# Kernel optimization log

Measured on AMD Instinct MI355X. Metric: run time of the kernel, lower is better.

The kernel has to match this reference:

```python
import jax, jax.numpy as jnp
import numpy as np

B, T = 64, 512          # batch, input_size
VOCAB = 16              # Embedding(16, ...)
UNITS = 256             # embedding dim
H = 512                 # LSTM hidden units (hard-coded in module)
F = 64                  # num_features (dense output)


def _glorot(key, shape):
    lim = np.sqrt(6.0 / (shape[0] + shape[1]))
    return jax.random.uniform(key, shape, jnp.float32, -lim, lim)


def setup_inputs() -> dict:
    key = jax.random.key(0)
    ks = jax.random.split(key, 9)
    tokens = jax.random.randint(ks[0], (B, T), 0, VOCAB, dtype=jnp.int32)
    return {
        "tokens": tokens,
        "emb": _glorot(ks[1], (VOCAB, UNITS)),
        "W1": _glorot(ks[2], (UNITS, 4 * H)),
        "U1": _glorot(ks[3], (H, 4 * H)),
        "b1": jnp.zeros((4 * H,), jnp.float32),
        "W2": _glorot(ks[4], (H, 4 * H)),
        "U2": _glorot(ks[5], (H, 4 * H)),
        "b2": jnp.zeros((4 * H,), jnp.float32),
        "Wd": _glorot(ks[6], (H, F)),
        "bd": jnp.zeros((F,), jnp.float32),
    }


def _lstm(x, mask, W, U, b, return_sequences):
    # x: [B, T, D]; mask: [B, T] bool. Keras semantics: masked steps carry
    # previous h and c (state and output pass through unchanged).
    xT = jnp.swapaxes(x, 0, 1)      # [T, B, D]
    mT = jnp.swapaxes(mask, 0, 1)   # [T, B]
    h0 = jnp.zeros((x.shape[0], U.shape[0]), x.dtype)
    c0 = h0

    def step(carry, inp):
        h, c = carry
        xt, mt = inp
        z = xt @ W + h @ U + b                    # [B, 4H]
        i, f, g, o = jnp.split(z, 4, axis=-1)     # Keras gate order i,f,c,o
        i = jax.nn.sigmoid(i)
        f = jax.nn.sigmoid(f)
        o = jax.nn.sigmoid(o)
        c_new = f * c + i * jnp.tanh(g)
        h_new = o * jnp.tanh(c_new)
        m = mt[:, None]
        h_new = jnp.where(m, h_new, h)
        c_new = jnp.where(m, c_new, c)
        return (h_new, c_new), h_new

    (h_last, _), hs = jax.lax.scan(step, (h0, c0), (xT, mT))
    return jnp.swapaxes(hs, 0, 1) if return_sequences else h_last


def reference(tokens, emb, W1, U1, b1, W2, U2, b2, Wd, bd):
    mask = tokens != 0                 # mask_zero=True
    x = emb[tokens]                    # [B, T, UNITS]
    h1 = _lstm(x, mask, W1, U1, b1, return_sequences=True)   # [B, T, H]
    h2 = _lstm(h1, mask, W2, U2, b2, return_sequences=False)  # [B, H]
    return h2 @ Wd + bd                # [B, F]
```

## Files before the change

### kernel.cpp

```cpp
#include <hip/hip_runtime.h>

#define BB   64
#define TT   512
#define NVOC 16
#define KIN  256
#define HH   512
#define GG   2048
#define FF   64

#define NWG  256
#define NTHR 512
#define WGPG 64
#define NGRP 4
#define BPG  16

#define TAB1_OFF 0
#define H1_OFF   32768
#define H2_OFF   98304

__device__ __forceinline__ void wg_barrier(unsigned* ctr, unsigned target) {
  __syncthreads();
  if (threadIdx.x == 0) {
    __hip_atomic_fetch_add(ctr, 1u, __ATOMIC_RELEASE, __HIP_MEMORY_SCOPE_AGENT);
    while (__hip_atomic_load(ctr, __ATOMIC_ACQUIRE, __HIP_MEMORY_SCOPE_AGENT) < target) {
      __builtin_amdgcn_s_sleep(2);
    }
  }
  __syncthreads();
}

extern "C" __global__ void __launch_bounds__(NTHR, 2)
lstm_fused(const int* __restrict__ tokens, const float* __restrict__ emb,
           const float* __restrict__ W1, const float* __restrict__ U1,
           const float* __restrict__ b1, const float* __restrict__ W2,
           const float* __restrict__ U2, const float* __restrict__ b2,
           const float* __restrict__ Wd, const float* __restrict__ bd,
           float* __restrict__ out, float* __restrict__ wsf,
           unsigned* __restrict__ ctr)
{
  const int wg   = blockIdx.x;
  const int grp  = wg >> 6;
  const int cb   = wg & 63;
  const int tid  = threadIdx.x;
  const int kq   = tid >> 7;
  const int cell = tid & 127;
  const int bl   = cell >> 3;
  const int jl   = cell & 7;
  const int b    = grp * BPG + bl;
  const int jh   = cb * 8 + jl;
  const int colz = jh;

  float* tab1 = wsf + TAB1_OFF;
  float* h1b0 = wsf + H1_OFF;
  float* h1b1 = wsf + H1_OFF + BB * HH;
  float* h2b0 = wsf + H2_OFF;
  float* h2b1 = wsf + H2_OFF + BB * HH;

  __shared__ float zred[4][128][4];

  {
    int g0 = wg * NTHR + tid;
    if (g0 < NVOC * GG) {
      int v = g0 >> 11, col = g0 & (GG - 1);
      float acc = b1[col];
      const float* e = emb + v * KIN;
      const float* w = W1 + col;
      #pragma unroll 4
      for (int k = 0; k < KIN; ++k) acc += e[k] * w[(size_t)k * GG];
      tab1[g0] = acc;
      h1b0[g0] = 0.f;
      h2b0[g0] = 0.f;
    }
  }
  wg_barrier(&ctr[8], NWG);

  unsigned bt = 0;
  float c1 = 0.f, c2 = 0.f;

  for (int t = 0; t < TT; ++t) {
    float* h1r = (t & 1) ? h1b1 : h1b0;
    float* h1w = (t & 1) ? h1b0 : h1b1;
    float* h2r = (t & 1) ? h2b1 : h2b0;
    float* h2w = (t & 1) ? h2b0 : h2b1;

    {
      float z0 = 0.f, z1 = 0.f, z2 = 0.f, z3 = 0.f;
      const int k0 = kq * 128;
      const float4* h4 = reinterpret_cast<const float4*>(h1r + b * HH + k0);
      const float* up = U1 + (size_t)k0 * GG + colz;
      #pragma unroll 2
      for (int k4 = 0; k4 < 32; ++k4) {
        float4 hv = h4[k4];
        const float* u0 = up;
        z0 += hv.x*u0[0]; z1 += hv.x*u0[512]; z2 += hv.x*u0[1024]; z3 += hv.x*u0[1536]; u0 += GG;
        z0 += hv.y*u0[0]; z1 += hv.y*u0[512]; z2 += hv.y*u0[1024]; z3 += hv.y*u0[1536]; u0 += GG;
        z0 += hv.z*u0[0]; z1 += hv.z*u0[512]; z2 += hv.z*u0[1024]; z3 += hv.z*u0[1536]; u0 += GG;
        z0 += hv.w*u0[0]; z1 += hv.w*u0[512]; z2 += hv.w*u0[1024]; z3 += hv.w*u0[1536];
        up += 4 * GG;
      }
      zred[kq][cell][0] = z0; zred[kq][cell][1] = z1;
      zred[kq][cell][2] = z2; zred[kq][cell][3] = z3;
    }
    __syncthreads();
    if (kq == 0) {
      float z0 = zred[0][cell][0]+zred[1][cell][0]+zred[2][cell][0]+zred[3][cell][0];
      float z1 = zred[0][cell][1]+zred[1][cell][1]+zred[2][cell][1]+zred[3][cell][1];
      float z2 = zred[0][cell][2]+zred[1][cell][2]+zred[2][cell][2]+zred[3][cell][2];
      float z3 = zred[0][cell][3]+zred[1][cell][3]+zred[2][cell][3]+zred[3][cell][3];
      int tok = tokens[b * TT + t];
      const float* tb = tab1 + (size_t)tok * GG + colz;
      z0 += tb[0]; z1 += tb[512]; z2 += tb[1024]; z3 += tb[1536];
      float sig_i = 1.f / (1.f + expf(-z0));
      float sig_f = 1.f / (1.f + expf(-z1));
      float g_t   = tanhf(z2);
      float sig_o = 1.f / (1.f + expf(-z3));
      float cn = sig_f * c1 + sig_i * g_t;
      float hn = sig_o * tanhf(cn);
      if (tok == 0) { cn = c1; hn = h1r[b * HH + jh]; }
      c1 = cn;
      h1w[b * HH + jh] = hn;
    }
    bt += WGPG;
    wg_barrier(&ctr[grp], bt);

    {
      float z0 = 0.f, z1 = 0.f, z2 = 0.f, z3 = 0.f;
      const float* xin = (kq < 2) ? (h1w + b * HH) : (h2r + b * HH);
      const float* WW  = (kq < 2) ? W2 : U2;
      const int k0 = (kq & 1) * 256;
      const float4* h4 = reinterpret_cast<const float4*>(xin + k0);
      const float* up = WW + (size_t)k0 * GG + colz;
      #pragma unroll 2
      for (int k4 = 0; k4 < 64; ++k4) {
        float4 hv = h4[k4];
        const float* u0 = up;
        z0 += hv.x*u0[0]; z1 += hv.x*u0[512]; z2 += hv.x*u0[1024]; z3 += hv.x*u0[1536]; u0 += GG;
        z0 += hv.y*u0[0]; z1 += hv.y*u0[512]; z2 += hv.y*u0[1024]; z3 += hv.y*u0[1536]; u0 += GG;
        z0 += hv.z*u0[0]; z1 += hv.z*u0[512]; z2 += hv.z*u0[1024]; z3 += hv.z*u0[1536]; u0 += GG;
        z0 += hv.w*u0[0]; z1 += hv.w*u0[512]; z2 += hv.w*u0[1024]; z3 += hv.w*u0[1536];
        up += 4 * GG;
      }
      zred[kq][cell][0] = z0; zred[kq][cell][1] = z1;
      zred[kq][cell][2] = z2; zred[kq][cell][3] = z3;
    }
    __syncthreads();
    if (kq == 0) {
      float z0 = zred[0][cell][0]+zred[1][cell][0]+zred[2][cell][0]+zred[3][cell][0];
      float z1 = zred[0][cell][1]+zred[1][cell][1]+zred[2][cell][1]+zred[3][cell][1];
      float z2 = zred[0][cell][2]+zred[1][cell][2]+zred[2][cell][2]+zred[3][cell][2];
      float z3 = zred[0][cell][3]+zred[1][cell][3]+zred[2][cell][3]+zred[3][cell][3];
      int tok = tokens[b * TT + t];
      z0 += b2[colz]; z1 += b2[colz + 512]; z2 += b2[colz + 1024]; z3 += b2[colz + 1536];
      float sig_i = 1.f / (1.f + expf(-z0));
      float sig_f = 1.f / (1.f + expf(-z1));
      float g_t   = tanhf(z2);
      float sig_o = 1.f / (1.f + expf(-z3));
      float cn = sig_f * c2 + sig_i * g_t;
      float hn = sig_o * tanhf(cn);
      if (tok == 0) { cn = c2; hn = h2r[b * HH + jh]; }
      c2 = cn;
      h2w[b * HH + jh] = hn;
    }
    bt += WGPG;
    wg_barrier(&ctr[grp], bt);
  }

  if (cb < 4 && tid < 256) {
    int bo = grp * BPG + (cb << 2) + (tid >> 6);
    int f  = tid & 63;
    const float* hf = h2b0 + bo * HH;
    const float* wd = Wd + f;
    float acc = bd[f];
    #pragma unroll 4
    for (int k = 0; k < HH; ++k) acc += hf[k] * wd[(size_t)k * FF];
    out[bo * FF + f] = acc;
  }
}

extern "C" void kernel_launch(void* const* d_in, const int* in_sizes, int n_in,
                              void* d_out, int out_size, void* d_ws, size_t ws_size,
                              hipStream_t stream) {
  const int*   tokens = (const int*)  d_in[0];
  const float* emb    = (const float*)d_in[1];
  const float* W1     = (const float*)d_in[2];
  const float* U1     = (const float*)d_in[3];
  const float* b1     = (const float*)d_in[4];
  const float* W2     = (const float*)d_in[5];
  const float* U2     = (const float*)d_in[6];
  const float* b2     = (const float*)d_in[7];
  const float* Wd     = (const float*)d_in[8];
  const float* bd     = (const float*)d_in[9];
  float*    out = (float*)d_out;
  unsigned* ctr = (unsigned*)d_ws;
  float*    wsf = (float*)((char*)d_ws + 64);

  hipMemsetAsync(d_ws, 0, 64, stream);

  void* args[] = { &tokens, &emb, &W1, &U1, &b1, &W2, &U2, &b2, &Wd, &bd,
                   &out, &wsf, &ctr };
  hipLaunchCooperativeKernel((void*)lstm_fused, dim3(NWG), dim3(NTHR),
                             args, 0, stream);
}
```

Before: 32.39 ms.

## Keep per-workgroup weight slices resident in LDS and stage hidden state through shared memory

Each workgroup now owns 4 hidden columns (16 gate columns) for half the batch. It loads its slices of U1, W2 and U2 into LDS once, along with a per-workgroup token table and bias, instead of streaming the weights from global or L2 every timestep. Hidden-state chunks are double-staged into swizzled LDS with register prefetch, and each thread computes 8 batch rows by 16-row K slices, followed by an 8-way LDS reduction. Barrier groups change from 4 groups of 64 workgroups to 2 groups of 128. The trade-offs are roughly 150KB of LDS per workgroup, many more __syncthreads per step, and larger grid barriers.

```diff
diff --git a/kernel.cpp b/kernel.cpp
--- a/kernel.cpp
+++ b/kernel.cpp
@@ -10,13 +10,21 @@
 
 #define NWG  256
 #define NTHR 512
-#define WGPG 64
-#define NGRP 4
-#define BPG  16
-
-#define TAB1_OFF 0
-#define H1_OFF   32768
-#define H2_OFF   98304
+
+#define U1W_OFF  0
+#define W2W_OFF  8384
+#define U2W_OFF  16768
+#define HLDS_OFF 25152
+#define ZRED_OFF 33344
+#define TABW_OFF 37696
+#define B2W_OFF  37952
+#define LDS_FLOATS 37968
+#define LDS_BYTES  (LDS_FLOATS * 4)
+
+#define H1A_OFF 0
+#define H1B_OFF 32768
+#define H2A_OFF 65536
+#define H2B_OFF 98304
 
 __device__ __forceinline__ void wg_barrier(unsigned* ctr, unsigned target) {
   __syncthreads();
@@ -29,151 +37,212 @@
   __syncthreads();
 }
 
+__device__ __forceinline__ void stage_ld(float4 v[4], const float* __restrict__ src, int tid) {
+  #pragma unroll
+  for (int jj = 0; jj < 4; ++jj) {
+    int f4 = jj * 512 + tid;
+    int b = f4 >> 6, k4l = f4 & 63;
+    v[jj] = *reinterpret_cast<const float4*>(src + b * HH + k4l * 4);
+  }
+}
+__device__ __forceinline__ void stage_st(float* __restrict__ hlds, const float4 v[4], int tid) {
+  float4* h4 = reinterpret_cast<float4*>(hlds);
+  #pragma unroll
+  for (int jj = 0; jj < 4; ++jj) {
+    int f4 = jj * 512 + tid;
+    int b = f4 >> 6, k4l = f4 & 63;
+    h4[b * 64 + (k4l ^ (b >> 3))] = v[jj];
+  }
+}
+
+__device__ __forceinline__ void inner8(float acc[8], const float* __restrict__ wrow,
+                                       const float4* __restrict__ h4base, int kq8, int bg) {
+  #pragma unroll
+  for (int j = 0; j < 8; ++j) {
+    int k4 = kq8 + j;
+    float4 w = *reinterpret_cast<const float4*>(wrow + k4 * 4);
+    const float4* hb = h4base + (k4 ^ bg);
+    float4 h0 = hb[0 * 64], h1 = hb[1 * 64], h2 = hb[2 * 64], h3 = hb[3 * 64];
+    float4 h4v = hb[4 * 64], h5 = hb[5 * 64], h6 = hb[6 * 64], h7 = hb[7 * 64];
+    acc[0] += h0.x * w.x; acc[0] += h0.y * w.y; acc[0] += h0.z * w.z; acc[0] += h0.w * w.w;
+    acc[1] += h1.x * w.x; acc[1] += h1.y * w.y; acc[1] += h1.z * w.z; acc[1] += h1.w * w.w;
+    acc[2] += h2.x * w.x; acc[2] += h2.y * w.y; acc[2] += h2.z * w.z; acc[2] += h2.w * w.w;
+    acc[3] += h3.x * w.x; acc[3] += h3.y * w.y; acc[3] += h3.z * w.z; acc[3] += h3.w * w.w;
+    acc[4] += h4v.x * w.x; acc[4] += h4v.y * w.y; acc[4] += h4v.z * w.z; acc[4] += h4v.w * w.w;
+    acc[5] += h5.x * w.x; acc[5] += h5.y * w.y; acc[5] += h5.z * w.z; acc[5] += h5.w * w.w;
+    acc[6] += h6.x * w.x; acc[6] += h6.y * w.y; acc[6] += h6.z * w.z; acc[6] += h6.w * w.w;
+    acc[7] += h7.x * w.x; acc[7] += h7.y * w.y; acc[7] += h7.z * w.z; acc[7] += h7.w * w.w;
+  }
+}
+
 extern "C" __global__ void __launch_bounds__(NTHR, 2)
-lstm_fused(const int* __restrict__ tokens, const float* __restrict__ emb,
-           const float* __restrict__ W1, const float* __restrict__ U1,
-           const float* __restrict__ b1, const float* __restrict__ W2,
-           const float* __restrict__ U2, const float* __restrict__ b2,
-           const float* __restrict__ Wd, const float* __restrict__ bd,
-           float* __restrict__ out, float* __restrict__ wsf,
-           unsigned* __restrict__ ctr)
+lstm_fused2(const int* __restrict__ tokens, const float* __restrict__ emb,
+            const float* __restrict__ W1, const float* __restrict__ U1,
+            const float* __restrict__ b1, const float* __restrict__ W2,
+            const float* __restrict__ U2, const float* __restrict__ b2,
+            const float* __restrict__ Wd, const float* __restrict__ bd,
+            float* __restrict__ out, float* __restrict__ wsf,
+            unsigned* __restrict__ ctr)
 {
-  const int wg   = blockIdx.x;
-  const int grp  = wg >> 6;
-  const int cb   = wg & 63;
-  const int tid  = threadIdx.x;
-  const int kq   = tid >> 7;
-  const int cell = tid & 127;
-  const int bl   = cell >> 3;
-  const int jl   = cell & 7;
-  const int b    = grp * BPG + bl;
-  const int jh   = cb * 8 + jl;
-  const int colz = jh;
-
-  float* tab1 = wsf + TAB1_OFF;
-  float* h1b0 = wsf + H1_OFF;
-  float* h1b1 = wsf + H1_OFF + BB * HH;
-  float* h2b0 = wsf + H2_OFF;
-  float* h2b1 = wsf + H2_OFF + BB * HH;
-
-  __shared__ float zred[4][128][4];
+  extern __shared__ float lds[];
+  float* u1w  = lds + U1W_OFF;
+  float* w2w  = lds + W2W_OFF;
+  float* u2w  = lds + U2W_OFF;
+  float* hlds = lds + HLDS_OFF;
+  float* zred = lds + ZRED_OFF;
+  float* tabw = lds + TABW_OFF;
+  float* b2w  = lds + B2W_OFF;
+
+  const int wg  = blockIdx.x;
+  const int tid = threadIdx.x;
+  const int bh  = wg >> 7;
+  const int ct  = wg & 127;
+  const int hc0 = ct * 4;
+  const int zcl = tid & 15;
+  const int bg  = (tid >> 4) & 3;
+  const int kq  = tid >> 6;
+  const int kq8 = kq * 8;
+
+  float* h1A = wsf + H1A_OFF; float* h1B = wsf + H1B_OFF;
+  float* h2A = wsf + H2A_OFF; float* h2B = wsf + H2B_OFF;
 
   {
-    int g0 = wg * NTHR + tid;
-    if (g0 < NVOC * GG) {
-      int v = g0 >> 11, col = g0 & (GG - 1);
-      float acc = b1[col];
-      const float* e = emb + v * KIN;
-      const float* w = W1 + col;
-      #pragma unroll 4
-      for (int k = 0; k < KIN; ++k) acc += e[k] * w[(size_t)k * GG];
-      tab1[g0] = acc;
-      h1b0[g0] = 0.f;
-      h2b0[g0] = 0.f;
-    }
-  }
-  wg_barrier(&ctr[8], NWG);
-
-  unsigned bt = 0;
-  float c1 = 0.f, c2 = 0.f;
+    int k = tid;
+    #pragma unroll
+    for (int g = 0; g < 4; ++g) {
+      float4 a = *reinterpret_cast<const float4*>(U1 + (size_t)k * GG + hc0 + 512 * g);
+      u1w[(g * 4 + 0) * 524 + k] = a.x; u1w[(g * 4 + 1) * 524 + k] = a.y;
+      u1w[(g * 4 + 2) * 524 + k] = a.z; u1w[(g * 4 + 3) * 524 + k] = a.w;
+      float4 b_ = *reinterpret_cast<const float4*>(W2 + (size_t)k * GG + hc0 + 512 * g);
+      w2w[(g * 4 + 0) * 524 + k] = b_.x; w2w[(g * 4 + 1) * 524 + k] = b_.y;
+      w2w[(g * 4 + 2) * 524 + k] = b_.z; w2w[(g * 4 + 3) * 524 + k] = b_.w;
+      float4 c_ = *reinterpret_cast<const float4*>(U2 + (size_t)k * GG + hc0 + 512 * g);
+      u2w[(g * 4 + 0) * 524 + k] = c_.x; u2w[(g * 4 + 1) * 524 + k] = c_.y;
+      u2w[(g * 4 + 2) * 524 + k] = c_.z; u2w[(g * 4 + 3) * 524 + k] = c_.w;
+    }
+  }
+  if (tid < 256) {
+    int v = tid >> 4, zz = tid & 15;
+    int col = hc0 + (zz & 3) + ((zz >> 2) << 9);
+    float a = b1[col];
+    #pragma unroll 4
+    for (int k = 0; k < KIN; ++k) a += emb[v * KIN + k] * W1[(size_t)k * GG + col];
+    tabw[v * 16 + zz] = a;
+  }
+  if (tid < 16) b2w[tid] = b2[hc0 + (tid & 3) + ((tid >> 2) << 9)];
+  {
+    if (tid < 128)       h1A[bh * 16384 + ct * 128 + tid] = 0.f;
+    else if (tid < 256)  h2A[bh * 16384 + ct * 128 + (tid - 128)] = 0.f;
+  }
+  unsigned bt = 128;
+  wg_barrier(&ctr[bh], bt);
+
+  float c1 = 0.f, hp1 = 0.f, c2 = 0.f, hp2 = 0.f;
+  const int fb = tid >> 2;
+  const int fc = tid & 3;
+
+  const float4* h4base = reinterpret_cast<const float4*>(hlds) + bg * 512;
+  const float* u1row = u1w + zcl * 524;
+  const float* w2row = w2w + zcl * 524;
+  const float* u2row = u2w + zcl * 524;
 
   for (int t = 0; t < TT; ++t) {
-    float* h1r = (t & 1) ? h1b1 : h1b0;
-    float* h1w = (t & 1) ? h1b0 : h1b1;
-    float* h2r = (t & 1) ? h2b1 : h2b0;
-    float* h2w = (t & 1) ? h2b0 : h2b1;
-
-    {
-      float z0 = 0.f, z1 = 0.f, z2 = 0.f, z3 = 0.f;
-      const int k0 = kq * 128;
-      const float4* h4 = reinterpret_cast<const float4*>(h1r + b * HH + k0);
-      const float* up = U1 + (size_t)k0 * GG + colz;
-      #pragma unroll 2
-      for (int k4 = 0; k4 < 32; ++k4) {
-        float4 hv = h4[k4];
-        const float* u0 = up;
-        z0 += hv.x*u0[0]; z1 += hv.x*u0[512]; z2 += hv.x*u0[1024]; z3 += hv.x*u0[1536]; u0 += GG;
-        z0 += hv.y*u0[0]; z1 += hv.y*u0[512]; z2 += hv.y*u0[1024]; z3 += hv.y*u0[1536]; u0 += GG;
-        z0 += hv.z*u0[0]; z1 += hv.z*u0[512]; z2 += hv.z*u0[1024]; z3 += hv.z*u0[1536]; u0 += GG;
-        z0 += hv.w*u0[0]; z1 += hv.w*u0[512]; z2 += hv.w*u0[1024]; z3 += hv.w*u0[1536];
-        up += 4 * GG;
+    float* h1r = (t & 1) ? h1B : h1A;
+    float* h1w = (t & 1) ? h1A : h1B;
+    float* h2r = (t & 1) ? h2B : h2A;
+    float* h2w = (t & 1) ? h2A : h2B;
+    const float* h1r_half = h1r + bh * 32 * HH;
+    const float* h2r_half = h2r + bh * 32 * HH;
+    const float* h1w_half = h1w + bh * 32 * HH;
+
+    float acc[8] = {0,0,0,0,0,0,0,0};
+    float4 pre[4];
+
+    stage_ld(pre, h1r_half, tid);
+    __syncthreads(); stage_st(hlds, pre, tid); __syncthreads();
+    stage_ld(pre, h1r_half + 256, tid);
+    inner8(acc, u1row, h4base, kq8, bg);
+    __syncthreads(); stage_st(hlds, pre, tid); __syncthreads();
+    stage_ld(pre, h2r_half, tid);
+    inner8(acc, u1row + 256, h4base, kq8, bg);
+
+    __syncthreads();
+    #pragma unroll
+    for (int i = 0; i < 8; ++i) zred[kq * 544 + (bg * 8 + i) * 17 + zcl] = acc[i];
+    __syncthreads();
+    if (tid < 128) {
+      float z[4];
+      #pragma unroll
+      for (int g = 0; g < 4; ++g) {
+        float s = 0.f;
+        #pragma unroll
+        for (int q = 0; q < 8; ++q) s += zred[q * 544 + fb * 17 + g * 4 + fc];
+        z[g] = s;
       }
-      zred[kq][cell][0] = z0; zred[kq][cell][1] = z1;
-      zred[kq][cell][2] = z2; zred[kq][cell][3] = z3;
-    }
-    __syncthreads();
-    if (kq == 0) {
-      float z0 = zred[0][cell][0]+zred[1][cell][0]+zred[2][cell][0]+zred[3][cell][0];
-      float z1 = zred[0][cell][1]+zred[1][cell][1]+zred[2][cell][1]+zred[3][cell][1];
-      float z2 = zred[0][cell][2]+zred[1][cell][2]+zred[2][cell][2]+zred[3][cell][2];
-      float z3 = zred[0][cell][3]+zred[1][cell][3]+zred[2][cell][3]+zred[3][cell][3];
-      int tok = tokens[b * TT + t];
-      const float* tb = tab1 + (size_t)tok * GG + colz;
-      z0 += tb[0]; z1 += tb[512]; z2 += tb[1024]; z3 += tb[1536];
-      float sig_i = 1.f / (1.f + expf(-z0));
-      float sig_f = 1.f / (1.f + expf(-z1));
-      float g_t   = tanhf(z2);
-      float sig_o = 1.f / (1.f + expf(-z3));
-      float cn = sig_f * c1 + sig_i * g_t;
-      float hn = sig_o * tanhf(cn);
-      if (tok == 0) { cn = c1; hn = h1r[b * HH + jh]; }
-      c1 = cn;
-      h1w[b * HH + jh] = hn;
-    }
-    bt += WGPG;
-    wg_barrier(&ctr[grp], bt);
-
-    {
-      float z0 = 0.f, z1 = 0.f, z2 = 0.f, z3 = 0.f;
-      const float* xin = (kq < 2) ? (h1w + b * HH) : (h2r + b * HH);
-      const float* WW  = (kq < 2) ? W2 : U2;
-      const int k0 = (kq & 1) * 256;
-      const float4* h4 = reinterpret_cast<const float4*>(xin + k0);
-      const float* up = WW + (size_t)k0 * GG + colz;
-      #pragma unroll 2
-      for (int k4 = 0; k4 < 64; ++k4) {
-        float4 hv = h4[k4];
-        const float* u0 = up;
-        z0 += hv.x*u0[0]; z1 += hv.x*u0[512]; z2 += hv.x*u0[1024]; z3 += hv.x*u0[1536]; u0 += GG;
-        z0 += hv.y*u0[0]; z1 += hv.y*u0[512]; z2 += hv.y*u0[1024]; z3 += hv.y*u0[1536]; u0 += GG;
-        z0 += hv.z*u0[0]; z1 += hv.z*u0[512]; z2 += hv.z*u0[1024]; z3 += hv.z*u0[1536]; u0 += GG;
-        z0 += hv.w*u0[0]; z1 += hv.w*u0[512]; z2 += hv.w*u0[1024]; z3 += hv.w*u0[1536];
-        up += 4 * GG;
+      int tok = tokens[(bh * 32 + fb) * TT + t];
+      #pragma unroll
+      for (int g = 0; g < 4; ++g) z[g] += tabw[tok * 16 + g * 4 + fc];
+      float si = 1.f / (1.f + expf(-z[0]));
+      float sf = 1.f / (1.f + expf(-z[1]));
+      float gg = tanhf(z[2]);
+      float so = 1.f / (1.f + expf(-z[3]));
+      float cn = sf * c1 + si * gg;
+      float hn = so * tanhf(cn);
+      if (tok == 0) { cn = c1; hn = hp1; }
+      c1 = cn; hp1 = hn;
+      h1w[(bh * 32 + fb) * HH + hc0 + fc] = hn;
+    }
+    bt += 128; wg_barrier(&ctr[bh], bt);
+
+    #pragma unroll
+    for (int i = 0; i < 8; ++i) acc[i] = 0.f;
+    __syncthreads(); stage_st(hlds, pre, tid); __syncthreads();
+    stage_ld(pre, h2r_half + 256, tid);
+    inner8(acc, u2row, h4base, kq8, bg);
+    __syncthreads(); stage_st(hlds, pre, tid); __syncthreads();
+    stage_ld(pre, h1w_half, tid);
+    inner8(acc, u2row + 256, h4base, kq8, bg);
+    __syncthreads(); stage_st(hlds, pre, tid); __syncthreads();
+    stage_ld(pre, h1w_half + 256, tid);
+    inner8(acc, w2row, h4base, kq8, bg);
+    __syncthreads(); stage_st(hlds, pre, tid); __syncthreads();
+    inner8(acc, w2row + 256, h4base, kq8, bg);
+
+    __syncthreads();
+    #pragma unroll
+    for (int i = 0; i < 8; ++i) zred[kq * 544 + (bg * 8 + i) * 17 + zcl] = acc[i];
+    __syncthreads();
+    if (tid < 128) {
+      float z[4];
+      #pragma unroll
+      for (int g = 0; g < 4; ++g) {
+        float s = 0.f;
+        #pragma unroll
+        for (int q = 0; q < 8; ++q) s += zred[q * 544 + fb * 17 + g * 4 + fc];
+        z[g] = s + b2w[g * 4 + fc];
       }
-      zred[kq][cell][0] = z0; zred[kq][cell][1] = z1;
-      zred[kq][cell][2] = z2; zred[kq][cell][3] = z3;
-    }
-    __syncthreads();
-    if (kq == 0) {
-      float z0 = zred[0][cell][0]+zred[1][cell][0]+zred[2][cell][0]+zred[3][cell][0];
-      float z1 = zred[0][cell][1]+zred[1][cell][1]+zred[2][cell][1]+zred[3][cell][1];
-      float z2 = zred[0][cell][2]+zred[1][cell][2]+zred[2][cell][2]+zred[3][cell][2];
-      float z3 = zred[0][cell][3]+zred[1][cell][3]+zred[2][cell][3]+zred[3][cell][3];
-      int tok = tokens[b * TT + t];
-      z0 += b2[colz]; z1 += b2[colz + 512]; z2 += b2[colz + 1024]; z3 += b2[colz + 1536];
-      float sig_i = 1.f / (1.f + expf(-z0));
-      float sig_f = 1.f / (1.f + expf(-z1));
-      float g_t   = tanhf(z2);
-      float sig_o = 1.f / (1.f + expf(-z3));
-      float cn = sig_f * c2 + sig_i * g_t;
-      float hn = sig_o * tanhf(cn);
-      if (tok == 0) { cn = c2; hn = h2r[b * HH + jh]; }
-      c2 = cn;
-      h2w[b * HH + jh] = hn;
-    }
-    bt += WGPG;
-    wg_barrier(&ctr[grp], bt);
-  }
-
-  if (cb < 4 && tid < 256) {
-    int bo = grp * BPG + (cb << 2) + (tid >> 6);
-    int f  = tid & 63;
-    const float* hf = h2b0 + bo * HH;
-    const float* wd = Wd + f;
-    float acc = bd[f];
-    #pragma unroll 4
-    for (int k = 0; k < HH; ++k) acc += hf[k] * wd[(size_t)k * FF];
-    out[bo * FF + f] = acc;
+      int tok = tokens[(bh * 32 + fb) * TT + t];
+      float si = 1.f / (1.f + expf(-z[0]));
+      float sf = 1.f / (1.f + expf(-z[1]));
+      float gg = tanhf(z[2]);
+      float so = 1.f / (1.f + expf(-z[3]));
+      float cn = sf * c2 + si * gg;
+      float hn = so * tanhf(cn);
+      if (tok == 0) { cn = c2; hn = hp2; }
+      c2 = cn; hp2 = hn;
+      h2w[(bh * 32 + fb) * HH + hc0 + fc] = hn;
+    }
+    bt += 128; wg_barrier(&ctr[bh], bt);
+  }
+
+  if (ct < 4) {
+    int idx = ct * 512 + tid;
+    int b = idx >> 6, f = idx & 63;
+    const float* hf = h2A + (bh * 32 + b) * HH;
+    float a = bd[f];
+    #pragma unroll 8
+    for (int k = 0; k < HH; ++k) a += hf[k] * Wd[(size_t)k * FF + f];
+    out[(bh * 32 + b) * FF + f] = a;
   }
 }
 
@@ -194,10 +263,13 @@
   unsigned* ctr = (unsigned*)d_ws;
   float*    wsf = (float*)((char*)d_ws + 64);
 
+  hipFuncSetAttribute((const void*)lstm_fused2,
+                      hipFuncAttributeMaxDynamicSharedMemorySize, LDS_BYTES);
+
   hipMemsetAsync(d_ws, 0, 64, stream);
 
   void* args[] = { &tokens, &emb, &W1, &U1, &b1, &W2, &U2, &b2, &Wd, &bd,
                    &out, &wsf, &ctr };
-  hipLaunchCooperativeKernel((void*)lstm_fused, dim3(NWG), dim3(NTHR),
-                             args, 0, stream);
-}
+  hipLaunchCooperativeKernel((void*)lstm_fused2, dim3(NWG), dim3(NTHR),
+                             args, LDS_BYTES, stream);
+}
```

Result: faster. 28.02 ms (-13.5%).
